# Kernel optimization log

Hardware: AMD Instinct MI355X
Metric: run time of the kernel (lower is better)

Reference implementation:

```python
import jax, jax.numpy as jnp
import numpy as np
import math

B, S, H, NH, HD, RD, INNER, MAXPOS, EPS = 2, 2048, 4096, 16, 256, 64, 16384, 2048, 1e-5


def setup_inputs() -> dict:
    key = jax.random.key(0)
    ks = jax.random.split(key, 8)
    sd = 0.02
    return {
        "hidden_states": jax.random.normal(ks[0], (B, S, H), jnp.float32),
        "attention_mask": jnp.ones((B, S), jnp.int32),
        "position_ids": jnp.broadcast_to(jnp.arange(S, dtype=jnp.int32), (B, S)),
        "ln_scale": jnp.ones((H,), jnp.float32),
        "ln_bias": jnp.zeros((H,), jnp.float32),
        "wq": jax.random.normal(ks[1], (H, H), jnp.float32) * sd,
        "wk": jax.random.normal(ks[2], (H, H), jnp.float32) * sd,
        "wv": jax.random.normal(ks[3], (H, H), jnp.float32) * sd,
        "wo": jax.random.normal(ks[4], (H, H), jnp.float32) * sd,
        "w_in": jax.random.normal(ks[5], (H, INNER), jnp.float32) * sd,
        "b_in": jnp.zeros((INNER,), jnp.float32),
        "w_out": jax.random.normal(ks[6], (INNER, H), jnp.float32) * sd,
        "b_out": jnp.zeros((H,), jnp.float32),
    }


def _rotate_every_two(t):
    # interleave (-odd, even) pairs along last dim
    r = jnp.stack((-t[..., 1::2], t[..., ::2]), axis=-1)
    return r.reshape(t.shape)


def reference(hidden_states, attention_mask, position_ids, ln_scale, ln_bias,
              wq, wk, wv, wo, w_in, b_in, w_out, b_out):
    x = hidden_states
    # LayerNorm (single ln feeds both attn and mlp in GPT-J parallel block)
    mu = jnp.mean(x, axis=-1, keepdims=True)
    var = jnp.mean(jnp.square(x - mu), axis=-1, keepdims=True)
    h = (x - mu) * jax.lax.rsqrt(var + EPS) * ln_scale + ln_bias

    # QKV projections (no bias), split heads: [B,S,NH,HD]
    q = (h @ wq).reshape(B, S, NH, HD)
    k = (h @ wk).reshape(B, S, NH, HD)
    v = (h @ wv).reshape(B, S, NH, HD)

    # sinusoidal table over rotary_dim, gathered by position_ids
    pos = jnp.arange(MAXPOS, dtype=jnp.float32)
    inv_freq = 1.0 / (10000.0 ** (jnp.arange(0, RD, 2, dtype=jnp.float32) / RD))
    freqs = pos[:, None] * inv_freq[None, :]          # [MAXPOS, RD//2]
    table = jnp.concatenate([jnp.sin(freqs), jnp.cos(freqs)], axis=-1)  # [MAXPOS, RD]
    sincos = table[position_ids]                      # [B,S,RD]
    sin, cos = jnp.split(sincos, 2, axis=-1)          # each [B,S,RD//2]
    sinr = jnp.repeat(sin[:, :, None, :], 2, axis=3)  # [B,S,1,RD]
    cosr = jnp.repeat(cos[:, :, None, :], 2, axis=3)

    def rope(t):
        return t * cosr + _rotate_every_two(t) * sinr

    q = jnp.concatenate([rope(q[..., :RD]), q[..., RD:]], axis=-1)
    k = jnp.concatenate([rope(k[..., :RD]), k[..., RD:]], axis=-1)

    # combined causal + padding mask -> additive bias
    causal = jnp.tril(jnp.ones((S, S), dtype=bool))
    mask = (attention_mask[:, None, None, :] > 0) & causal[None, None, :, :]
    bias = jnp.where(mask, 0.0, jnp.finfo(jnp.float32).min)  # [B,1,S,S]

    scale = 1.0 / math.sqrt(HD)
    scores = jnp.einsum('bqhd,bkhd->bhqk', q, k) * scale + bias
    attn = jax.nn.softmax(scores, axis=-1)
    ctx = jnp.einsum('bhqk,bkhd->bqhd', attn, v).reshape(B, S, H)
    attn_out = ctx @ wo

    # MLP on the same LN output (parallel residual), gelu_new ~ tanh gelu
    mlp = jax.nn.gelu(h @ w_in + b_in, approximate=True) @ w_out + b_out

    return x + attn_out + mlp
```

## Files before the change

kernel.cpp:

```cpp
#include <hip/hip_runtime.h>
#include <hip/hip_bf16.h>
#include <math.h>

namespace {

constexpr int kB = 2;
constexpr int kS = 2048;
constexpr int kH = 4096;
constexpr int kNH = 16;
constexpr int kHD = 256;

typedef __attribute__((ext_vector_type(4))) float f32x4;
typedef __attribute__((ext_vector_type(8))) short bf16x8;

__device__ __forceinline__ unsigned short f2bf(float f) {
  unsigned int u = __float_as_uint(f);
  u += 0x7FFFu + ((u >> 16) & 1u);
  return (unsigned short)(u >> 16);
}
__device__ __forceinline__ float bf2f(unsigned short h) {
  return __uint_as_float(((unsigned int)h) << 16);
}
__device__ __forceinline__ void gl2lds16(const void* g, void* l) {
  __builtin_amdgcn_global_load_lds(
      (const __attribute__((address_space(1))) unsigned int*)g,
      (__attribute__((address_space(3))) unsigned int*)l, 16, 0, 0);
}

__global__ __launch_bounds__(256) void ln_fwd(
    const float* __restrict__ x, const float* __restrict__ gam,
    const float* __restrict__ bet, unsigned short* __restrict__ hout,
    float* __restrict__ outp) {
  int row = blockIdx.x;
  int t = threadIdx.x;
  const float4* xr = (const float4*)(x + (size_t)row * kH);
  float4 v[4];
  float sum = 0.f, sq = 0.f;
#pragma unroll
  for (int i = 0; i < 4; i++) {
    v[i] = xr[t + i * 256];
    sum += v[i].x + v[i].y + v[i].z + v[i].w;
    sq += v[i].x * v[i].x + v[i].y * v[i].y + v[i].z * v[i].z + v[i].w * v[i].w;
  }
#pragma unroll
  for (int o = 32; o > 0; o >>= 1) {
    sum += __shfl_xor(sum, o);
    sq += __shfl_xor(sq, o);
  }
  __shared__ float red[8];
  if ((t & 63) == 0) { red[t >> 6] = sum; red[4 + (t >> 6)] = sq; }
  __syncthreads();
  sum = red[0] + red[1] + red[2] + red[3];
  sq = red[4] + red[5] + red[6] + red[7];
  float mu = sum * (1.f / kH);
  float rstd = rsqrtf(sq * (1.f / kH) - mu * mu + 1e-5f);
  const float4* gp = (const float4*)gam;
  const float4* bp = (const float4*)bet;
  ushort4* hr = (ushort4*)(hout + (size_t)row * kH);
  float4* orow = (float4*)(outp + (size_t)row * kH);
#pragma unroll
  for (int i = 0; i < 4; i++) {
    float4 g = gp[t + i * 256];
    float4 bb = bp[t + i * 256];
    ushort4 hv;
    hv.x = f2bf((v[i].x - mu) * rstd * g.x + bb.x);
    hv.y = f2bf((v[i].y - mu) * rstd * g.y + bb.y);
    hv.z = f2bf((v[i].z - mu) * rstd * g.z + bb.z);
    hv.w = f2bf((v[i].w - mu) * rstd * g.w + bb.w);
    hr[t + i * 256] = hv;
    orow[t + i * 256] = v[i];
  }
}

__global__ __launch_bounds__(256) void cvt_t(
    const float* __restrict__ in, int ldin, unsigned short* __restrict__ outp,
    int ldout) {
  __shared__ float tile[32][33];
  int n0 = blockIdx.x * 32, k0 = blockIdx.y * 32;
  int tx = threadIdx.x, ty = threadIdx.y;
#pragma unroll
  for (int i = 0; i < 4; i++)
    tile[ty + i * 8][tx] = in[(size_t)(k0 + ty + i * 8) * ldin + n0 + tx];
  __syncthreads();
#pragma unroll
  for (int i = 0; i < 4; i++)
    outp[(size_t)(n0 + ty + i * 8) * ldout + k0 + tx] =
        f2bf(tile[tx][ty + i * 8]);
}

__global__ __launch_bounds__(256) void vtrans(
    const unsigned short* __restrict__ v, unsigned short* __restrict__ vt) {
  __shared__ unsigned short tile[32][33];
  int bh = blockIdx.z;
  int s0 = blockIdx.x * 32, d0 = blockIdx.y * 32;
  int tx = threadIdx.x, ty = threadIdx.y;
  int b = bh >> 4, h = bh & 15;
  const unsigned short* src = v + (size_t)(b * kS) * kH + h * kHD;
#pragma unroll
  for (int i = 0; i < 4; i++)
    tile[ty + i * 8][tx] = src[(size_t)(s0 + ty + i * 8) * kH + d0 + tx];
  __syncthreads();
  unsigned short* dst = vt + (size_t)bh * kHD * kS;
#pragma unroll
  for (int i = 0; i < 4; i++)
    dst[(size_t)(d0 + ty + i * 8) * kS + s0 + tx] = tile[tx][ty + i * 8];
}

__global__ __launch_bounds__(256) void rope_scale(
    unsigned short* __restrict__ q, unsigned short* __restrict__ k,
    const int* __restrict__ pos) {
  int idx = blockIdx.x * 256 + threadIdx.x;
  int j = idx & 127;
  int rowh = idx >> 7;
  int h = rowh & 15;
  int s = (rowh >> 4) & 2047;
  int b = rowh >> 15;
  size_t off = ((size_t)(b * kS + s)) * kH + h * kHD + 2 * j;
  const float SCALE = 0.0625f;
  if (j < 32) {
    int p = pos[b * kS + s];
    float inv = exp2f(-(float)j * (13.287712379549449f / 32.f));
    float fr = (float)p * inv;
    float sn, cs;
    sincosf(fr, &sn, &cs);
    float e = bf2f(q[off]), o = bf2f(q[off + 1]);
    q[off] = f2bf((e * cs - o * sn) * SCALE);
    q[off + 1] = f2bf((o * cs + e * sn) * SCALE);
    e = bf2f(k[off]); o = bf2f(k[off + 1]);
    k[off] = f2bf(e * cs - o * sn);
    k[off + 1] = f2bf(o * cs + e * sn);
  } else {
    q[off] = f2bf(bf2f(q[off]) * SCALE);
    q[off + 1] = f2bf(bf2f(q[off + 1]) * SCALE);
  }
}

#define AF_MMA(P)                                                           \
  {                                                                         \
    bf16x8 af_[2][2];                                                       \
    _Pragma("unroll") for (int fm = 0; fm < 2; fm++)                        \
        _Pragma("unroll") for (int kk = 0; kk < 2; kk++) {                  \
      int q_ = (2 * (P) + fm) * 16 + l15;                                   \
      af_[fm][kk] = *(const bf16x8*)(cur + ((q_ & 64) << 8) + wm * 8192 +   \
                                     ((q_ & 63) << 7) +                     \
                                     ((((kk << 2) | l4) ^ key) << 4));      \
    }                                                                       \
    asm volatile("s_barrier" ::: "memory");                                 \
    __builtin_amdgcn_s_setprio(1);                                          \
    _Pragma("unroll") for (int fm = 0; fm < 2; fm++)                        \
        _Pragma("unroll") for (int fn = 0; fn < 4; fn++)                    \
            _Pragma("unroll") for (int kk = 0; kk < 2; kk++)                \
      acc[2 * (P) + fm][fn] = __builtin_amdgcn_mfma_f32_16x16x32_bf16(      \
          af_[fm][kk], bfr[fn][kk], acc[2 * (P) + fm][fn], 0, 0, 0);        \
    __builtin_amdgcn_s_setprio(0);                                          \
  }

template <int EPI>
__global__ __launch_bounds__(512, 2) void gemm256(
    const unsigned short* __restrict__ A, int lda,
    const unsigned short* __restrict__ Bt, int ldb, void* __restrict__ Cp,
    int ldc, const float* __restrict__ bias, int K, int gx) {
  __shared__ __align__(16) char lds[131072];
  const int t = threadIdx.x;
  const int lane = t & 63, w = t >> 6;
  const int wm = w >> 2, wn = w & 3;
  const int l15 = lane & 15, l4 = lane >> 4;
  const int key = l15 & 7;

  const int nwg = gridDim.x;
  const int orig = blockIdx.x;
  const int wg = (orig & 7) * (nwg >> 3) + (orig >> 3);
  const int bx = wg % gx, by = wg / gx;
  const int m0 = by * 256, n0 = bx * 256;

  const int lr = t >> 3, ch = t & 7;
  const int swk = (ch ^ (lr & 7)) * 8;
  const unsigned short* aE0 = A + (size_t)(m0 + lr) * lda + swk;
  const unsigned short* aE1 = A + (size_t)(m0 + 128 + lr) * lda + swk;
  const unsigned short* aL0 = A + (size_t)(m0 + 64 + lr) * lda + swk;
  const unsigned short* aL1 = A + (size_t)(m0 + 192 + lr) * lda + swk;
  const unsigned short* b00 = Bt + (size_t)(n0 + lr) * ldb + swk;
  const unsigned short* b01 = Bt + (size_t)(n0 + 64 + lr) * ldb + swk;
  const unsigned short* b10 = Bt + (size_t)(n0 + 128 + lr) * ldb + swk;
  const unsigned short* b11 = Bt + (size_t)(n0 + 192 + lr) * ldb + swk;
  const int t16 = t * 16;

  f32x4 acc[8][4];
#pragma unroll
  for (int m = 0; m < 8; m++)
#pragma unroll
    for (int n = 0; n < 4; n++) acc[m][n] = (f32x4)(0.f);

  {
    char* b = lds;
    gl2lds16(b00, b + 32768 + t16); b00 += 64;
    gl2lds16(b01, b + 40960 + t16); b01 += 64;
    gl2lds16(b10, b + 49152 + t16); b10 += 64;
    gl2lds16(b11, b + 57344 + t16); b11 += 64;
    gl2lds16(aE0, b + t16);         aE0 += 64;
    gl2lds16(aE1, b + 8192 + t16);  aE1 += 64;
    gl2lds16(aL0, b + 16384 + t16); aL0 += 64;
    gl2lds16(aL1, b + 24576 + t16); aL1 += 64;
  }
  asm volatile("s_waitcnt vmcnt(0)" ::: "memory");
  asm volatile("s_barrier" ::: "memory");

  const int nt = K >> 6;
  for (int kt = 0; kt < nt; ++kt) {
    const char* cur = lds + (kt & 1) * 65536;
    char* nxt = lds + (((kt & 1) ^ 1)) * 65536;
    const bool pre = (kt + 1 < nt);
    bf16x8 bfr[4][2];
    if (pre) {
      gl2lds16(b00, nxt + 32768 + t16); b00 += 64;
      gl2lds16(b01, nxt + 40960 + t16); b01 += 64;
    }
#pragma unroll
    for (int fn = 0; fn < 4; fn++)
#pragma unroll
      for (int kk = 0; kk < 2; kk++) {
        int n = wn * 64 + fn * 16 + l15;
        bfr[fn][kk] = *(const bf16x8*)(cur + 32768 + (n << 7) +
                                       ((((kk << 2) | l4) ^ key) << 4));
      }
    AF_MMA(0)
    asm volatile("s_barrier" ::: "memory");
    if (pre) {
      gl2lds16(b10, nxt + 49152 + t16); b10 += 64;
      gl2lds16(b11, nxt + 57344 + t16); b11 += 64;
    }
    AF_MMA(1)
    if (pre) asm volatile("s_waitcnt vmcnt(4)" ::: "memory");
    else     asm volatile("s_waitcnt vmcnt(0)" ::: "memory");
    asm volatile("s_barrier" ::: "memory");
    if (pre) {
      gl2lds16(aE0, nxt + t16);        aE0 += 64;
      gl2lds16(aE1, nxt + 8192 + t16); aE1 += 64;
    }
    AF_MMA(2)
    asm volatile("s_barrier" ::: "memory");
    if (pre) {
      gl2lds16(aL0, nxt + 16384 + t16); aL0 += 64;
      gl2lds16(aL1, nxt + 24576 + t16); aL1 += 64;
    }
    AF_MMA(3)
    asm volatile("s_waitcnt lgkmcnt(0)" ::: "memory");
    if (pre) asm volatile("s_waitcnt vmcnt(2)" ::: "memory");
    asm volatile("s_barrier" ::: "memory");
  }

  const int crow = m0 + wm * 128 + l4 * 4;
  const int ccol = n0 + wn * 64 + l15;
#pragma unroll
  for (int m = 0; m < 8; m++) {
#pragma unroll
    for (int n = 0; n < 4; n++) {
      int col = ccol + n * 16;
#pragma unroll
      for (int r = 0; r < 4; r++) {
        int row = crow + m * 16 + r;
        float v = acc[m][n][r];
        size_t idx = (size_t)row * ldc + col;
        if constexpr (EPI == 0) {
          ((unsigned short*)Cp)[idx] = f2bf(v);
        } else if constexpr (EPI == 1) {
          float u = v + bias[col];
          float c = 0.7978845608028654f * (u + 0.044715f * u * u * u);
          float g = u / (1.0f + __expf(-2.0f * c));
          ((unsigned short*)Cp)[idx] = f2bf(g);
        } else if constexpr (EPI == 2) {
          ((float*)Cp)[idx] += v;
        } else {
          ((float*)Cp)[idx] += v + bias[col];
        }
      }
    }
  }
}

__global__ __launch_bounds__(256) void attn_fwd(
    const unsigned short* __restrict__ q, const unsigned short* __restrict__ k,
    const unsigned short* __restrict__ vt, const int* __restrict__ amask,
    unsigned short* __restrict__ ctx) {
  __shared__ unsigned short sK[32 * 256];
  __shared__ unsigned short sV[256 * 32];
  __shared__ unsigned short sP[4 * 16 * 32];
  int t = threadIdx.x, lane = t & 63, w = t >> 6;
  int qb = blockIdx.x, bh = blockIdx.y;
  int b = bh >> 4, h = bh & 15;
  int l15 = lane & 15, l4 = lane >> 4;

  bf16x8 qf[8];
  {
    int qrow = qb * 64 + w * 16 + l15;
    const unsigned short* qp =
        q + (size_t)(b * kS + qrow) * kH + h * kHD + l4 * 8;
#pragma unroll
    for (int ks = 0; ks < 8; ks++) qf[ks] = *(const bf16x8*)(qp + ks * 32);
  }
  f32x4 o[16];
#pragma unroll
  for (int nf = 0; nf < 16; nf++) o[nf] = (f32x4)(0.f);
  float mr[4] = {-INFINITY, -INFINITY, -INFINITY, -INFINITY};
  float lr[4] = {0.f, 0.f, 0.f, 0.f};

  int krow = t >> 5, kchk = t & 31;
  int vrow = t >> 2, vchk = t & 3;
  const unsigned short* kbase = k + (size_t)(b * kS) * kH + h * kHD;
  const unsigned short* vbase = vt + (size_t)bh * kHD * kS;
  int ntiles = 2 * qb + 2;

  for (int kvt = 0; kvt < ntiles; kvt++) {
    int kv0 = kvt * 32;
    __syncthreads();
#pragma unroll
    for (int i = 0; i < 4; i++) {
      int row = krow + i * 8;
      int csw = kchk ^ (row & 7);
      gl2lds16(kbase + (size_t)(kv0 + row) * kH + csw * 8,
               (char*)sK + i * 4096 + t * 16);
      int d = vrow + i * 64;
      int csw2 = vchk ^ ((d >> 1) & 3);
      gl2lds16(vbase + (size_t)d * kS + kv0 + csw2 * 8,
               (char*)sV + i * 4096 + t * 16);
    }
    __syncthreads();

    f32x4 sc[2];
    sc[0] = (f32x4)(0.f);
    sc[1] = (f32x4)(0.f);
#pragma unroll
    for (int nf = 0; nf < 2; nf++) {
      int row = nf * 16 + l15;
#pragma unroll
      for (int ks = 0; ks < 8; ks++) {
        int slot = (ks * 4 + l4) ^ (row & 7);
        bf16x8 kf = *(const bf16x8*)&sK[row * 256 + slot * 8];
        sc[nf] = __builtin_amdgcn_mfma_f32_16x16x32_bf16(qf[ks], kf, sc[nf], 0, 0, 0);
      }
    }

    int am0 = amask[b * kS + kv0 + l15];
    int am1 = amask[b * kS + kv0 + 16 + l15];
    int kva = kv0 + l15, kvb = kv0 + 16 + l15;
#pragma unroll
    for (int r = 0; r < 4; r++) {
      int qi = qb * 64 + w * 16 + l4 * 4 + r;
      float s0v = (kva <= qi && am0 != 0) ? sc[0][r] : -INFINITY;
      float s1v = (kvb <= qi && am1 != 0) ? sc[1][r] : -INFINITY;
      float mx = fmaxf(s0v, s1v);
#pragma unroll
      for (int d = 1; d < 16; d <<= 1) mx = fmaxf(mx, __shfl_xor(mx, d));
      float mn = fmaxf(mr[r], mx);
      float corr = __expf(mr[r] - mn);
      float p0 = __expf(s0v - mn);
      float p1 = __expf(s1v - mn);
      float rsum = p0 + p1;
#pragma unroll
      for (int d = 1; d < 16; d <<= 1) rsum += __shfl_xor(rsum, d);
      lr[r] = lr[r] * corr + rsum;
      mr[r] = mn;
#pragma unroll
      for (int nf = 0; nf < 16; nf++) o[nf][r] *= corr;
      int prow = l4 * 4 + r;
      int swz = ((prow >> 1) & 3) << 4;
      int byte0 = prow * 64 + ((l15 * 2) ^ swz);
      int byte1 = prow * 64 + (((16 + l15) * 2) ^ swz);
      sP[w * 512 + (byte0 >> 1)] = f2bf(p0);
      sP[w * 512 + (byte1 >> 1)] = f2bf(p1);
    }

    int pslot = l4 ^ ((l15 >> 1) & 3);
    bf16x8 pa = *(const bf16x8*)&sP[w * 512 + l15 * 32 + pslot * 8];
#pragma unroll
    for (int nf = 0; nf < 16; nf++) {
      int vr = nf * 16 + l15;
      int vslot = l4 ^ ((vr >> 1) & 3);
      bf16x8 vf = *(const bf16x8*)&sV[vr * 32 + vslot * 8];
      o[nf] = __builtin_amdgcn_mfma_f32_16x16x32_bf16(pa, vf, o[nf], 0, 0, 0);
    }
  }

  float invl[4];
#pragma unroll
  for (int r = 0; r < 4; r++) invl[r] = 1.0f / lr[r];
#pragma unroll
  for (int nf = 0; nf < 16; nf++) {
    int d = nf * 16 + l15;
#pragma unroll
    for (int r = 0; r < 4; r++) {
      int qi = qb * 64 + w * 16 + l4 * 4 + r;
      ctx[(size_t)(b * kS + qi) * kH + h * kHD + d] = f2bf(o[nf][r] * invl[r]);
    }
  }
}

}

extern "C" void kernel_launch(void* const* d_in, const int* in_sizes, int n_in,
                              void* d_out, int out_size, void* d_ws,
                              size_t ws_size, hipStream_t stream) {
  const float* x = (const float*)d_in[0];
  const int* amask = (const int*)d_in[1];
  const int* pos = (const int*)d_in[2];
  const float* lns = (const float*)d_in[3];
  const float* lnb = (const float*)d_in[4];
  const float* wq = (const float*)d_in[5];
  const float* wk = (const float*)d_in[6];
  const float* wv = (const float*)d_in[7];
  const float* wo = (const float*)d_in[8];
  const float* w_in = (const float*)d_in[9];
  const float* b_in = (const float*)d_in[10];
  const float* w_out = (const float*)d_in[11];
  const float* b_out = (const float*)d_in[12];
  float* out = (float*)d_out;

  if (ws_size < 268435456ull) return;
  char* ws = (char*)d_ws;
  unsigned short* h_bf = (unsigned short*)ws;
  unsigned short* big = (unsigned short*)(ws + 33554432ull);
  unsigned short* vbuf = (unsigned short*)(ws + 167772160ull);
  unsigned short* wbuf = (unsigned short*)(ws + 201326592ull);
  unsigned short* mid = big;
  unsigned short* qbuf = big;
  unsigned short* kbuf = big + 16777216;
  unsigned short* vtb = big + 33554432;
  unsigned short* ctxb = vbuf;

  dim3 t256(256);
  dim3 t512(512);
  dim3 t32x8(32, 8);

  ln_fwd<<<kB * kS, t256, 0, stream>>>(x, lns, lnb, h_bf, out);

  for (int c = 0; c < 2; c++) {
    cvt_t<<<dim3(256, 128), t32x8, 0, stream>>>(w_in + c * 8192, 16384, wbuf, 4096);
    gemm256<1><<<dim3(512), t512, 0, stream>>>(
        h_bf, 4096, wbuf, 4096, mid + c * 8192, 16384, b_in + c * 8192, 4096, 32);
  }
  for (int c = 0; c < 2; c++) {
    cvt_t<<<dim3(128, 256), t32x8, 0, stream>>>(
        w_out + (size_t)c * 8192 * 4096, 4096, wbuf, 8192);
    if (c == 0)
      gemm256<3><<<dim3(256), t512, 0, stream>>>(mid + c * 8192, 16384, wbuf,
                                                 8192, out, 4096, b_out, 8192, 16);
    else
      gemm256<2><<<dim3(256), t512, 0, stream>>>(
          mid + c * 8192, 16384, wbuf, 8192, out, 4096, nullptr, 8192, 16);
  }

  const float* wqkv[3] = {wq, wk, wv};
  unsigned short* qkvp[3] = {qbuf, kbuf, vbuf};
  for (int i = 0; i < 3; i++) {
    cvt_t<<<dim3(128, 128), t32x8, 0, stream>>>(wqkv[i], 4096, wbuf, 4096);
    gemm256<0><<<dim3(256), t512, 0, stream>>>(h_bf, 4096, wbuf, 4096,
                                               qkvp[i], 4096, nullptr, 4096, 16);
  }
  rope_scale<<<32768, t256, 0, stream>>>(qbuf, kbuf, pos);
  vtrans<<<dim3(64, 8, 32), t32x8, 0, stream>>>(vbuf, vtb);
  attn_fwd<<<dim3(32, 32), t256, 0, stream>>>(qbuf, kbuf, vtb, amask, ctxb);
  cvt_t<<<dim3(128, 128), t32x8, 0, stream>>>(wo, 4096, wbuf, 4096);
  gemm256<2><<<dim3(256), t512, 0, stream>>>(ctxb, 4096, wbuf, 4096, out,
                                             4096, nullptr, 4096, 16);
}
```

Before: 2.289 ms.

## Restructure attention kernel with double-buffered KV tiles and lazy softmax rescale

The attention kernel now uses 512-thread blocks covering 128 query rows and 64-key KV tiles. K and V tiles are double-buffered in LDS with asynchronous global-to-LDS loads, so the next tile is fetched while the current one is computed. Blocks are ordered heaviest-first for causal load balance, and MFMA sections run at raised wave priority. The online softmax skips rescaling the output accumulator unless the running max grows by more than a threshold. The cost is about 144KB of LDS per block, which allows only one block per CU, and looser manual waitcnt/barrier synchronisation.

```diff
diff --git a/kernel.cpp b/kernel.cpp
--- a/kernel.cpp
+++ b/kernel.cpp
@@ -278,21 +278,22 @@
   }
 }
 
-__global__ __launch_bounds__(256) void attn_fwd(
+__global__ __launch_bounds__(512) void attn_fwd(
     const unsigned short* __restrict__ q, const unsigned short* __restrict__ k,
     const unsigned short* __restrict__ vt, const int* __restrict__ amask,
     unsigned short* __restrict__ ctx) {
-  __shared__ unsigned short sK[32 * 256];
-  __shared__ unsigned short sV[256 * 32];
-  __shared__ unsigned short sP[4 * 16 * 32];
-  int t = threadIdx.x, lane = t & 63, w = t >> 6;
-  int qb = blockIdx.x, bh = blockIdx.y;
-  int b = bh >> 4, h = bh & 15;
-  int l15 = lane & 15, l4 = lane >> 4;
+  __shared__ __align__(16) char alds[147456];
+  const int t = threadIdx.x, lane = t & 63, w = t >> 6;
+  const int bid = blockIdx.x;
+  const int qb = 15 - (bid >> 5);
+  const int bh = bid & 31;
+  const int b = bh >> 4, h = bh & 15;
+  const int l15 = lane & 15, l4 = lane >> 4;
+  const int qbase = qb * 128;
 
   bf16x8 qf[8];
   {
-    int qrow = qb * 64 + w * 16 + l15;
+    int qrow = qbase + w * 16 + l15;
     const unsigned short* qp =
         q + (size_t)(b * kS + qrow) * kH + h * kHD + l4 * 8;
 #pragma unroll
@@ -304,81 +305,131 @@
   float mr[4] = {-INFINITY, -INFINITY, -INFINITY, -INFINITY};
   float lr[4] = {0.f, 0.f, 0.f, 0.f};
 
-  int krow = t >> 5, kchk = t & 31;
-  int vrow = t >> 2, vchk = t & 3;
   const unsigned short* kbase = k + (size_t)(b * kS) * kH + h * kHD;
   const unsigned short* vbase = vt + (size_t)bh * kHD * kS;
-  int ntiles = 2 * qb + 2;
-
-  for (int kvt = 0; kvt < ntiles; kvt++) {
-    int kv0 = kvt * 32;
-    __syncthreads();
-#pragma unroll
-    for (int i = 0; i < 4; i++) {
-      int row = krow + i * 8;
-      int csw = kchk ^ (row & 7);
-      gl2lds16(kbase + (size_t)(kv0 + row) * kH + csw * 8,
-               (char*)sK + i * 4096 + t * 16);
-      int d = vrow + i * 64;
-      int csw2 = vchk ^ ((d >> 1) & 3);
-      gl2lds16(vbase + (size_t)d * kS + kv0 + csw2 * 8,
-               (char*)sV + i * 4096 + t * 16);
-    }
-    __syncthreads();
-
-    f32x4 sc[2];
-    sc[0] = (f32x4)(0.f);
-    sc[1] = (f32x4)(0.f);
-#pragma unroll
-    for (int nf = 0; nf < 2; nf++) {
-      int row = nf * 16 + l15;
+  unsigned short* sPw = (unsigned short*)(alds + 131072 + w * 2048);
+  const int nt = 2 * qb + 2;
+
+  const int krow = t >> 5, kch = t & 31;
+  const int kcs = (kch ^ (krow & 7)) * 8;
+  const int vrow = t >> 3, vch = t & 7;
+  const int vcs = (vch ^ (vrow & 7)) * 8;
+  const int t16b = t * 16;
+
+#define ATTN_STAGE(KV0, BUF)                                                 \
+  {                                                                          \
+    char* kd = alds + (BUF) * 32768;                                         \
+    char* vd = alds + 65536 + (BUF) * 32768;                                 \
+    _Pragma("unroll") for (int i = 0; i < 4; i++) {                          \
+      gl2lds16(kbase + (size_t)((KV0) + krow + i * 16) * kH + kcs,           \
+               kd + i * 8192 + t16b);                                        \
+      gl2lds16(vbase + (size_t)(vrow + i * 64) * kS + (KV0) + vcs,           \
+               vd + i * 8192 + t16b);                                        \
+    }                                                                        \
+  }
+
+  ATTN_STAGE(0, 0)
+
+  for (int kvt = 0; kvt < nt; kvt++) {
+    const int kv0 = kvt * 64;
+    const int cb = kvt & 1;
+    if (kvt + 1 < nt) {
+      ATTN_STAGE(kv0 + 64, cb ^ 1)
+      asm volatile("s_waitcnt vmcnt(8)" ::: "memory");
+    } else {
+      asm volatile("s_waitcnt vmcnt(0)" ::: "memory");
+    }
+    asm volatile("s_barrier" ::: "memory");
+
+    const unsigned short* sK = (const unsigned short*)(alds + cb * 32768);
+    const unsigned short* sV =
+        (const unsigned short*)(alds + 65536 + cb * 32768);
+
+    f32x4 sc[4];
+#pragma unroll
+    for (int g = 0; g < 4; g++) sc[g] = (f32x4)(0.f);
+    __builtin_amdgcn_s_setprio(1);
+#pragma unroll
+    for (int g = 0; g < 4; g++) {
+      int row = g * 16 + l15;
 #pragma unroll
       for (int ks = 0; ks < 8; ks++) {
-        int slot = (ks * 4 + l4) ^ (row & 7);
-        bf16x8 kf = *(const bf16x8*)&sK[row * 256 + slot * 8];
-        sc[nf] = __builtin_amdgcn_mfma_f32_16x16x32_bf16(qf[ks], kf, sc[nf], 0, 0, 0);
-      }
-    }
-
-    int am0 = amask[b * kS + kv0 + l15];
-    int am1 = amask[b * kS + kv0 + 16 + l15];
-    int kva = kv0 + l15, kvb = kv0 + 16 + l15;
+        bf16x8 kf =
+            *(const bf16x8*)&sK[row * 256 + (((ks * 4 + l4) ^ (row & 7)) * 8)];
+        sc[g] = __builtin_amdgcn_mfma_f32_16x16x32_bf16(qf[ks], kf, sc[g], 0, 0, 0);
+      }
+    }
+    __builtin_amdgcn_s_setprio(0);
+
+    int am[4];
+#pragma unroll
+    for (int g = 0; g < 4; g++) am[g] = amask[b * kS + kv0 + g * 16 + l15];
+    float mx[4];
 #pragma unroll
     for (int r = 0; r < 4; r++) {
-      int qi = qb * 64 + w * 16 + l4 * 4 + r;
-      float s0v = (kva <= qi && am0 != 0) ? sc[0][r] : -INFINITY;
-      float s1v = (kvb <= qi && am1 != 0) ? sc[1][r] : -INFINITY;
-      float mx = fmaxf(s0v, s1v);
-#pragma unroll
-      for (int d = 1; d < 16; d <<= 1) mx = fmaxf(mx, __shfl_xor(mx, d));
-      float mn = fmaxf(mr[r], mx);
-      float corr = __expf(mr[r] - mn);
-      float p0 = __expf(s0v - mn);
-      float p1 = __expf(s1v - mn);
-      float rsum = p0 + p1;
-#pragma unroll
-      for (int d = 1; d < 16; d <<= 1) rsum += __shfl_xor(rsum, d);
-      lr[r] = lr[r] * corr + rsum;
-      mr[r] = mn;
-#pragma unroll
-      for (int nf = 0; nf < 16; nf++) o[nf][r] *= corr;
+      int qi = qbase + w * 16 + l4 * 4 + r;
+      float a = -INFINITY;
+#pragma unroll
+      for (int g = 0; g < 4; g++) {
+        bool ok = (kv0 + g * 16 + l15 <= qi) && (am[g] != 0);
+        float s = ok ? sc[g][r] : -INFINITY;
+        sc[g][r] = s;
+        a = fmaxf(a, s);
+      }
+#pragma unroll
+      for (int d = 1; d < 16; d <<= 1) a = fmaxf(a, __shfl_xor(a, d));
+      mx[r] = a;
+    }
+    bool nd = false;
+#pragma unroll
+    for (int r = 0; r < 4; r++) nd |= (mx[r] > mr[r] + 8.f);
+    if (__any(nd)) {
+#pragma unroll
+      for (int r = 0; r < 4; r++) {
+        float nm = fmaxf(mr[r], mx[r]);
+        float c = __expf(mr[r] - nm);
+        lr[r] *= c;
+        mr[r] = nm;
+#pragma unroll
+        for (int nf = 0; nf < 16; nf++) o[nf][r] *= c;
+      }
+    }
+#pragma unroll
+    for (int r = 0; r < 4; r++) {
       int prow = l4 * 4 + r;
-      int swz = ((prow >> 1) & 3) << 4;
-      int byte0 = prow * 64 + ((l15 * 2) ^ swz);
-      int byte1 = prow * 64 + (((16 + l15) * 2) ^ swz);
-      sP[w * 512 + (byte0 >> 1)] = f2bf(p0);
-      sP[w * 512 + (byte1 >> 1)] = f2bf(p1);
-    }
-
-    int pslot = l4 ^ ((l15 >> 1) & 3);
-    bf16x8 pa = *(const bf16x8*)&sP[w * 512 + l15 * 32 + pslot * 8];
+      int pkey = (prow ^ (prow >> 2)) & 7;
+      float rs = 0.f;
+#pragma unroll
+      for (int g = 0; g < 4; g++) {
+        float p = __expf(sc[g][r] - mr[r]);
+        rs += p;
+        int kvl = g * 16 + l15;
+        sPw[prow * 64 + (((kvl >> 3) ^ pkey) << 3) + (kvl & 7)] = f2bf(p);
+      }
+#pragma unroll
+      for (int d = 1; d < 16; d <<= 1) rs += __shfl_xor(rs, d);
+      lr[r] += rs;
+    }
+    asm volatile("s_waitcnt lgkmcnt(0)" ::: "memory");
+
+    int rkey = (l15 ^ (l15 >> 2)) & 7;
+    bf16x8 pa[2];
+#pragma unroll
+    for (int ks2 = 0; ks2 < 2; ks2++)
+      pa[ks2] = *(const bf16x8*)&sPw[l15 * 64 + (((ks2 * 4 + l4) ^ rkey) << 3)];
+    __builtin_amdgcn_s_setprio(1);
 #pragma unroll
     for (int nf = 0; nf < 16; nf++) {
       int vr = nf * 16 + l15;
-      int vslot = l4 ^ ((vr >> 1) & 3);
-      bf16x8 vf = *(const bf16x8*)&sV[vr * 32 + vslot * 8];
-      o[nf] = __builtin_amdgcn_mfma_f32_16x16x32_bf16(pa, vf, o[nf], 0, 0, 0);
-    }
+#pragma unroll
+      for (int ks2 = 0; ks2 < 2; ks2++) {
+        bf16x8 vf =
+            *(const bf16x8*)&sV[vr * 64 + (((ks2 * 4 + l4) ^ (vr & 7)) * 8)];
+        o[nf] = __builtin_amdgcn_mfma_f32_16x16x32_bf16(pa[ks2], vf, o[nf], 0, 0, 0);
+      }
+    }
+    __builtin_amdgcn_s_setprio(0);
+    asm volatile("s_barrier" ::: "memory");
   }
 
   float invl[4];
@@ -389,10 +440,11 @@
     int d = nf * 16 + l15;
 #pragma unroll
     for (int r = 0; r < 4; r++) {
-      int qi = qb * 64 + w * 16 + l4 * 4 + r;
+      int qi = qbase + w * 16 + l4 * 4 + r;
       ctx[(size_t)(b * kS + qi) * kH + h * kHD + d] = f2bf(o[nf][r] * invl[r]);
     }
   }
+#undef ATTN_STAGE
 }
 
 }
@@ -458,7 +510,7 @@
   }
   rope_scale<<<32768, t256, 0, stream>>>(qbuf, kbuf, pos);
   vtrans<<<dim3(64, 8, 32), t32x8, 0, stream>>>(vbuf, vtb);
-  attn_fwd<<<dim3(32, 32), t256, 0, stream>>>(qbuf, kbuf, vtb, amask, ctxb);
+  attn_fwd<<<dim3(512), t512, 0, stream>>>(qbuf, kbuf, vtb, amask, ctxb);
   cvt_t<<<dim3(128, 128), t32x8, 0, stream>>>(wo, 4096, wbuf, 4096);
   gemm256<2><<<dim3(256), t512, 0, stream>>>(ctxb, 4096, wbuf, 4096, out,
                                              4096, nullptr, 4096, 16);
```

Result: faster. 2.080 ms (-9.1%).
